# Performance work log

Hardware: AMD Instinct MI355X
Metric: run time of the kernel (lower is better)

## Reference

```python
import jax, jax.numpy as jnp
import numpy as np

EPS = 1e-06


def setup_inputs() -> dict:
    key = jax.random.key(0)
    k1, k2 = jax.random.split(key)
    x = jax.random.normal(k1, (16, 64, 256, 256), dtype=jnp.float32)
    gamma = jax.random.normal(k2, (1,), dtype=jnp.float32)
    return {"x": x, "gamma": gamma}


def reference(x, gamma):
    B, C, H, W = x.shape
    N = H * W
    v = x.reshape(B, C, N)                      # Q = K = V = flattened x
    # l2_norm: normalize across channel dim (dim=-2) per spatial position
    inv_norm = 1.0 / (jnp.linalg.norm(v, axis=1) + 1e-06)   # [B, N]
    qn = v * inv_norm[:, None, :]               # [B, C, N], Q and K normalized identically
    q_sum = jnp.sum(qn, axis=1)                 # [B, N] (sum over channels)
    # tailor_sum: 1 / (N + K^T-summed-Q + eps) -> [B, C]
    tailor = 1.0 / (N + jnp.einsum('bcn,bn->bc', qn, q_sum) + EPS)
    value_sum = jnp.sum(v, axis=1)[:, None, :]  # [B, 1, N], broadcasts over C
    matrix = jnp.einsum('bcn,bmn->bcm', v, qn)  # V @ K^T : [B, C, C]
    matrix_sum = value_sum + jnp.einsum('bcm,bmn->bcn', matrix, qn)  # [B, C, N]
    weight_value = matrix_sum * tailor[:, :, None]
    return x + gamma * weight_value.reshape(B, C, H, W)
```

## Files before the change

kernel.cpp:

```cpp
#include <hip/hip_runtime.h>
#include <stdint.h>

#define BATCH 16
#define CDIM 64
#define NDIM 65536
#define EPSV 1e-6f

typedef __attribute__((ext_vector_type(8))) short bf16x8;
typedef __attribute__((ext_vector_type(4))) short bf16x4;
typedef __attribute__((ext_vector_type(4))) float f32x4;

static __device__ __forceinline__ uint32_t f2bf(float f) {
    uint32_t u = __builtin_bit_cast(uint32_t, f);
    return (u + 0x7fffu + ((u >> 16) & 1u)) >> 16;
}
static __device__ __forceinline__ float bf2f(uint32_t h) {
    uint32_t u = h << 16;
    return __builtin_bit_cast(float, u);
}

#define T1 256
#define P1 264
#define CHUNKS 4
#define NTILE1 64

__global__ __launch_bounds__(256, 4)
void gram_kernel(const float* __restrict__ x, float* __restrict__ pmat,
                 float* __restrict__ pt) {
    __shared__ __align__(16) short ldsU[CDIM][P1];
    __shared__ __align__(16) float ldsG[T1];
    __shared__ float red[4][CDIM];

    const int tid = threadIdx.x;
    const int b = blockIdx.x >> 6;
    const int tileIdx = blockIdx.x & 63;
    const int w = tid >> 6;
    const int lane = tid & 63;
    const int cq = lane >> 4;
    const int cr = lane & 15;

    f32x4 acc0 = {0.f, 0.f, 0.f, 0.f};
    f32x4 acc1 = acc0, acc2 = acc0, acc3 = acc0;
    float tpart = 0.f;

    const float* xbase = x + (size_t)b * CDIM * NDIM;

    for (int chunk = 0; chunk < CHUNKS; ++chunk) {
        const int n0 = tileIdx * (T1 * CHUNKS) + chunk * T1;
        const float* xb = xbase + n0 + tid;
        float ss = 0.f, cs = 0.f;
#pragma unroll 8
        for (int c = 0; c < CDIM; ++c) {
            float v = xb[(size_t)c * NDIM];
            ss += v * v;
            cs += v;
            ldsU[c][tid] = (short)f2bf(v);
        }
        const float inv = 1.f / (sqrtf(ss) + EPSV);
        const float sq = sqrtf(inv);
        ldsG[tid] = inv * sq * cs;
#pragma unroll 8
        for (int c = 0; c < CDIM; ++c) {
            uint32_t h = (uint16_t)ldsU[c][tid];
            ldsU[c][tid] = (short)f2bf(bf2f(h) * sq);
        }
        __syncthreads();
#pragma unroll
        for (int ks = 0; ks < 8; ++ks) {
            const int k0 = ks * 32 + cq * 8;
            bf16x8 afrag = *(const bf16x8*)&ldsU[w * 16 + cr][k0];
            bf16x8 b0 = *(const bf16x8*)&ldsU[cr][k0];
            bf16x8 b1 = *(const bf16x8*)&ldsU[16 + cr][k0];
            bf16x8 b2 = *(const bf16x8*)&ldsU[32 + cr][k0];
            bf16x8 b3 = *(const bf16x8*)&ldsU[48 + cr][k0];
            acc0 = __builtin_amdgcn_mfma_f32_16x16x32_bf16(afrag, b0, acc0, 0, 0, 0);
            acc1 = __builtin_amdgcn_mfma_f32_16x16x32_bf16(afrag, b1, acc1, 0, 0, 0);
            acc2 = __builtin_amdgcn_mfma_f32_16x16x32_bf16(afrag, b2, acc2, 0, 0, 0);
            acc3 = __builtin_amdgcn_mfma_f32_16x16x32_bf16(afrag, b3, acc3, 0, 0, 0);
        }
#pragma unroll
        for (int i = 0; i < 8; ++i) {
            const int nb = w * 64 + i * 8;
            bf16x8 uf = *(const bf16x8*)&ldsU[lane][nb];
            f32x4 g0 = *(const f32x4*)&ldsG[nb];
            f32x4 g1 = *(const f32x4*)&ldsG[nb + 4];
#pragma unroll
            for (int j = 0; j < 4; ++j) {
                tpart += bf2f((uint32_t)(uint16_t)uf[j]) * g0[j];
                tpart += bf2f((uint32_t)(uint16_t)uf[j + 4]) * g1[j];
            }
        }
        __syncthreads();
    }
    red[w][lane] = tpart;
    __syncthreads();
    if (tid < CDIM) {
        pt[(size_t)blockIdx.x * CDIM + tid] =
            red[0][tid] + red[1][tid] + red[2][tid] + red[3][tid];
    }
    float* pm = pmat + (size_t)blockIdx.x * CDIM * CDIM;
    const f32x4 accs[4] = {acc0, acc1, acc2, acc3};
#pragma unroll
    for (int mt = 0; mt < 4; ++mt) {
#pragma unroll
        for (int r = 0; r < 4; ++r) {
            const int row = w * 16 + cq * 4 + r;
            const int col = mt * 16 + cr;
            pm[row * CDIM + col] = accs[mt][r];
        }
    }
}

__global__ __launch_bounds__(256, 4)
void reduce_kernel(const float* __restrict__ pmat, const float* __restrict__ pt,
                   float* __restrict__ mat, float* __restrict__ tl) {
    const int blk = blockIdx.x;
    const int tid = threadIdx.x;
    if (blk < 256) {
        const int b = blk >> 4;
        const int o = (blk & 15) * 256 + tid;
        float s = 0.f;
#pragma unroll 8
        for (int t = 0; t < NTILE1; ++t)
            s += pmat[((size_t)(b * NTILE1 + t)) * (CDIM * CDIM) + o];
        mat[b * CDIM * CDIM + o] = s;
    } else {
        const int idx = (blk - 256) * 256 + tid;
        const int b = idx >> 6;
        const int c = idx & 63;
        float s = 0.f;
#pragma unroll 8
        for (int t = 0; t < NTILE1; ++t)
            s += pt[(size_t)(b * NTILE1 + t) * CDIM + c];
        tl[idx] = 1.f / ((float)NDIM + s + EPSV);
    }
}

#define T2 256
#define P2 68
#define PM 72

__global__ __launch_bounds__(256, 3)
void out_kernel(const float* __restrict__ x, const float* __restrict__ mat,
                const float* __restrict__ tl, const float* __restrict__ gamma,
                float* __restrict__ out) {
    __shared__ __align__(16) short ldsV[T2][P2];
    __shared__ __align__(16) short ldsM[CDIM][PM];
    __shared__ float ldsCS[T2];
    __shared__ float ldsIN[T2];
    __shared__ float ldsTL[CDIM];

    const int tid = threadIdx.x;
    const int bid = (int)(gridDim.x - 1 - blockIdx.x);
    const int b = bid >> 8;
    const int n0 = (bid & 255) * T2;
    const int w = tid >> 6;
    const int lane = tid & 63;
    const int cq = lane >> 4;
    const int cr = lane & 15;

    const float* mb = mat + (size_t)b * CDIM * CDIM;
#pragma unroll
    for (int i = 0; i < 16; ++i) {
        const int idx = tid + i * 256;
        ldsM[idx >> 6][idx & 63] = (short)f2bf(mb[idx]);
    }
    if (tid < CDIM) ldsTL[tid] = tl[b * CDIM + tid];

    const float* xb = x + (size_t)b * CDIM * NDIM + n0 + tid;
    float ss = 0.f, cs = 0.f;
#pragma unroll 8
    for (int cp = 0; cp < 32; ++cp) {
        float v0 = xb[(size_t)(2 * cp) * NDIM];
        float v1 = xb[(size_t)(2 * cp + 1) * NDIM];
        ss += v0 * v0 + v1 * v1;
        cs += v0 + v1;
        *(uint32_t*)&ldsV[tid][2 * cp] = f2bf(v0) | (f2bf(v1) << 16);
    }
    ldsIN[tid] = 1.f / (sqrtf(ss) + EPSV);
    ldsCS[tid] = cs;
    __syncthreads();

    bf16x8 afrag[4][2];
#pragma unroll
    for (int ct = 0; ct < 4; ++ct)
#pragma unroll
        for (int ks = 0; ks < 2; ++ks)
            afrag[ct][ks] = *(const bf16x8*)&ldsM[ct * 16 + cr][ks * 32 + cq * 8];

    f32x4 acc[4][4];
#pragma unroll
    for (int p = 0; p < 4; ++p)
#pragma unroll
        for (int ct = 0; ct < 4; ++ct)
            acc[p][ct] = (f32x4){0.f, 0.f, 0.f, 0.f};

#pragma unroll
    for (int p = 0; p < 4; ++p) {
        const int n = (w * 4 + p) * 16 + cr;
#pragma unroll
        for (int ks = 0; ks < 2; ++ks) {
            const int k0 = ks * 32 + cq * 8;
            bf16x4 lo = *(const bf16x4*)&ldsV[n][k0];
            bf16x4 hi = *(const bf16x4*)&ldsV[n][k0 + 4];
            bf16x8 bfrag = __builtin_shufflevector(lo, hi, 0, 1, 2, 3, 4, 5, 6, 7);
#pragma unroll
            for (int ct = 0; ct < 4; ++ct)
                acc[p][ct] = __builtin_amdgcn_mfma_f32_16x16x32_bf16(
                    afrag[ct][ks], bfrag, acc[p][ct], 0, 0, 0);
        }
    }

    const float g = gamma[0];
    float* ob = out + (size_t)b * CDIM * NDIM + n0;
#pragma unroll
    for (int p = 0; p < 4; ++p) {
        const int n = (w * 4 + p) * 16 + cr;
        const float csn = ldsCS[n];
        const float invn = ldsIN[n];
#pragma unroll
        for (int ct = 0; ct < 4; ++ct) {
            const int c0 = ct * 16 + cq * 4;
            bf16x4 xv4 = *(const bf16x4*)&ldsV[n][c0];
#pragma unroll
            for (int r = 0; r < 4; ++r) {
                const int c = c0 + r;
                ob[(size_t)c * NDIM + n] =
                    bf2f((uint32_t)(uint16_t)xv4[r]) +
                    g * ldsTL[c] * (csn + invn * acc[p][ct][r]);
            }
        }
    }
}

extern "C" void kernel_launch(void* const* d_in, const int* in_sizes, int n_in,
                              void* d_out, int out_size, void* d_ws, size_t ws_size,
                              hipStream_t stream) {
    const float* x = (const float*)d_in[0];
    const float* gamma = (const float*)d_in[1];
    float* out = (float*)d_out;
    float* pmat = (float*)d_ws;
    float* pt = pmat + (size_t)1024 * CDIM * CDIM;
    float* mat = pt + (size_t)1024 * CDIM;
    float* tl = mat + BATCH * CDIM * CDIM;
    hipLaunchKernelGGL(gram_kernel, dim3(BATCH * NTILE1), dim3(256), 0, stream,
                       x, pmat, pt);
    hipLaunchKernelGGL(reduce_kernel, dim3(260), dim3(256), 0, stream,
                       pmat, pt, mat, tl);
    hipLaunchKernelGGL(out_kernel, dim3(BATCH * 256), dim3(256), 0, stream,
                       x, mat, tl, gamma, out);
}
```

Before: 552.4 us.

## Cache normalized fp16 U in workspace to avoid re-reading fp32 x

The gram kernel now writes the normalized, channel-contiguous fp16 U and per-position column sum and scale to workspace. The output kernel reads these instead of re-reading and re-normalizing fp32 x, reconstructing x from U. MFMA switches from bf16 to fp16, and non-temporal loads and stores are added. This cuts second-pass HBM traffic but reconstructs the residual from fp16, which loses precision, and adds extra workspace writes.

After: 534.1 us. -3.3%, faster.

```diff
diff --git a/kernel.cpp b/kernel.cpp
--- a/kernel.cpp
+++ b/kernel.cpp
@@ -6,17 +6,16 @@
 #define NDIM 65536
 #define EPSV 1e-6f
 
-typedef __attribute__((ext_vector_type(8))) short bf16x8;
-typedef __attribute__((ext_vector_type(4))) short bf16x4;
+typedef __attribute__((ext_vector_type(8))) _Float16 f16x8;
 typedef __attribute__((ext_vector_type(4))) float f32x4;
-
-static __device__ __forceinline__ uint32_t f2bf(float f) {
-    uint32_t u = __builtin_bit_cast(uint32_t, f);
-    return (u + 0x7fffu + ((u >> 16) & 1u)) >> 16;
-}
-static __device__ __forceinline__ float bf2f(uint32_t h) {
-    uint32_t u = h << 16;
-    return __builtin_bit_cast(float, u);
+typedef __attribute__((ext_vector_type(4))) uint32_t u32x4;
+typedef __attribute__((ext_vector_type(4))) short s16x4;
+
+static __device__ __forceinline__ short h2s(_Float16 h) {
+    return (short)__builtin_bit_cast(unsigned short, h);
+}
+static __device__ __forceinline__ _Float16 s2h(short s) {
+    return __builtin_bit_cast(_Float16, (unsigned short)s);
 }
 
 #define T1 256
@@ -26,7 +25,8 @@
 
 __global__ __launch_bounds__(256, 4)
 void gram_kernel(const float* __restrict__ x, float* __restrict__ pmat,
-                 float* __restrict__ pt) {
+                 float* __restrict__ pt, short* __restrict__ ut,
+                 float2* __restrict__ meta) {
     __shared__ __align__(16) short ldsU[CDIM][P1];
     __shared__ __align__(16) float ldsG[T1];
     __shared__ float red[4][CDIM];
@@ -47,47 +47,62 @@
 
     for (int chunk = 0; chunk < CHUNKS; ++chunk) {
         const int n0 = tileIdx * (T1 * CHUNKS) + chunk * T1;
-        const float* xb = xbase + n0 + tid;
+        const int n = n0 + tid;
+        const float* xb = xbase + n;
         float ss = 0.f, cs = 0.f;
 #pragma unroll 8
         for (int c = 0; c < CDIM; ++c) {
-            float v = xb[(size_t)c * NDIM];
+            float v = __builtin_nontemporal_load(xb + (size_t)c * NDIM);
             ss += v * v;
             cs += v;
-            ldsU[c][tid] = (short)f2bf(v);
+            ldsU[c][tid] = h2s((_Float16)v);
         }
         const float inv = 1.f / (sqrtf(ss) + EPSV);
         const float sq = sqrtf(inv);
+        const _Float16 sqh = (_Float16)sq;
         ldsG[tid] = inv * sq * cs;
-#pragma unroll 8
-        for (int c = 0; c < CDIM; ++c) {
-            uint32_t h = (uint16_t)ldsU[c][tid];
-            ldsU[c][tid] = (short)f2bf(bf2f(h) * sq);
+        meta[(size_t)b * NDIM + n] = make_float2(cs, (float)sqh);
+        short* urow = ut + ((size_t)b * NDIM + n) * CDIM;
+#pragma unroll
+        for (int c8 = 0; c8 < CDIM; c8 += 8) {
+            uint32_t pk0, pk1, pk2, pk3;
+#pragma unroll
+            for (int j = 0; j < 4; ++j) {
+                _Float16 u0 = s2h(ldsU[c8 + 2 * j][tid]) * sqh;
+                _Float16 u1 = s2h(ldsU[c8 + 2 * j + 1][tid]) * sqh;
+                ldsU[c8 + 2 * j][tid] = h2s(u0);
+                ldsU[c8 + 2 * j + 1][tid] = h2s(u1);
+                uint32_t p = (uint32_t)__builtin_bit_cast(unsigned short, u0) |
+                             ((uint32_t)__builtin_bit_cast(unsigned short, u1) << 16);
+                if (j == 0) pk0 = p; else if (j == 1) pk1 = p;
+                else if (j == 2) pk2 = p; else pk3 = p;
+            }
+            *(u32x4*)(urow + c8) = (u32x4){pk0, pk1, pk2, pk3};
         }
         __syncthreads();
 #pragma unroll
         for (int ks = 0; ks < 8; ++ks) {
             const int k0 = ks * 32 + cq * 8;
-            bf16x8 afrag = *(const bf16x8*)&ldsU[w * 16 + cr][k0];
-            bf16x8 b0 = *(const bf16x8*)&ldsU[cr][k0];
-            bf16x8 b1 = *(const bf16x8*)&ldsU[16 + cr][k0];
-            bf16x8 b2 = *(const bf16x8*)&ldsU[32 + cr][k0];
-            bf16x8 b3 = *(const bf16x8*)&ldsU[48 + cr][k0];
-            acc0 = __builtin_amdgcn_mfma_f32_16x16x32_bf16(afrag, b0, acc0, 0, 0, 0);
-            acc1 = __builtin_amdgcn_mfma_f32_16x16x32_bf16(afrag, b1, acc1, 0, 0, 0);
-            acc2 = __builtin_amdgcn_mfma_f32_16x16x32_bf16(afrag, b2, acc2, 0, 0, 0);
-            acc3 = __builtin_amdgcn_mfma_f32_16x16x32_bf16(afrag, b3, acc3, 0, 0, 0);
+            f16x8 afrag = *(const f16x8*)&ldsU[w * 16 + cr][k0];
+            f16x8 b0 = *(const f16x8*)&ldsU[cr][k0];
+            f16x8 b1 = *(const f16x8*)&ldsU[16 + cr][k0];
+            f16x8 b2 = *(const f16x8*)&ldsU[32 + cr][k0];
+            f16x8 b3 = *(const f16x8*)&ldsU[48 + cr][k0];
+            acc0 = __builtin_amdgcn_mfma_f32_16x16x32_f16(afrag, b0, acc0, 0, 0, 0);
+            acc1 = __builtin_amdgcn_mfma_f32_16x16x32_f16(afrag, b1, acc1, 0, 0, 0);
+            acc2 = __builtin_amdgcn_mfma_f32_16x16x32_f16(afrag, b2, acc2, 0, 0, 0);
+            acc3 = __builtin_amdgcn_mfma_f32_16x16x32_f16(afrag, b3, acc3, 0, 0, 0);
         }
 #pragma unroll
         for (int i = 0; i < 8; ++i) {
             const int nb = w * 64 + i * 8;
-            bf16x8 uf = *(const bf16x8*)&ldsU[lane][nb];
+            f16x8 uf = *(const f16x8*)&ldsU[lane][nb];
             f32x4 g0 = *(const f32x4*)&ldsG[nb];
             f32x4 g1 = *(const f32x4*)&ldsG[nb + 4];
 #pragma unroll
             for (int j = 0; j < 4; ++j) {
-                tpart += bf2f((uint32_t)(uint16_t)uf[j]) * g0[j];
-                tpart += bf2f((uint32_t)(uint16_t)uf[j + 4]) * g1[j];
+                tpart += (float)uf[j] * g0[j];
+                tpart += (float)uf[j + 4] * g1[j];
             }
         }
         __syncthreads();
@@ -113,7 +128,7 @@
 
 __global__ __launch_bounds__(256, 4)
 void reduce_kernel(const float* __restrict__ pmat, const float* __restrict__ pt,
-                   float* __restrict__ mat, float* __restrict__ tl) {
+                   short* __restrict__ matb, float* __restrict__ tl) {
     const int blk = blockIdx.x;
     const int tid = threadIdx.x;
     if (blk < 256) {
@@ -122,8 +137,9 @@
         float s = 0.f;
 #pragma unroll 8
         for (int t = 0; t < NTILE1; ++t)
-            s += pmat[((size_t)(b * NTILE1 + t)) * (CDIM * CDIM) + o];
-        mat[b * CDIM * CDIM + o] = s;
+            s += __builtin_nontemporal_load(
+                &pmat[((size_t)(b * NTILE1 + t)) * (CDIM * CDIM) + o]);
+        matb[(size_t)b * CDIM * CDIM + o] = h2s((_Float16)s);
     } else {
         const int idx = (blk - 256) * 256 + tid;
         const int b = idx >> 6;
@@ -131,62 +147,47 @@
         float s = 0.f;
 #pragma unroll 8
         for (int t = 0; t < NTILE1; ++t)
-            s += pt[(size_t)(b * NTILE1 + t) * CDIM + c];
+            s += __builtin_nontemporal_load(&pt[(size_t)(b * NTILE1 + t) * CDIM + c]);
         tl[idx] = 1.f / ((float)NDIM + s + EPSV);
     }
 }
 
-#define T2 256
-#define P2 68
 #define PM 72
 
 __global__ __launch_bounds__(256, 3)
-void out_kernel(const float* __restrict__ x, const float* __restrict__ mat,
-                const float* __restrict__ tl, const float* __restrict__ gamma,
-                float* __restrict__ out) {
-    __shared__ __align__(16) short ldsV[T2][P2];
+void out_kernel(const short* __restrict__ ut, const short* __restrict__ matb,
+                const float* __restrict__ tl, const float2* __restrict__ meta,
+                const float* __restrict__ gamma, float* __restrict__ out) {
     __shared__ __align__(16) short ldsM[CDIM][PM];
-    __shared__ float ldsCS[T2];
-    __shared__ float ldsIN[T2];
     __shared__ float ldsTL[CDIM];
 
     const int tid = threadIdx.x;
     const int bid = (int)(gridDim.x - 1 - blockIdx.x);
     const int b = bid >> 8;
-    const int n0 = (bid & 255) * T2;
+    const int n0 = (bid & 255) * 256;
     const int w = tid >> 6;
     const int lane = tid & 63;
     const int cq = lane >> 4;
     const int cr = lane & 15;
 
-    const float* mb = mat + (size_t)b * CDIM * CDIM;
-#pragma unroll
-    for (int i = 0; i < 16; ++i) {
-        const int idx = tid + i * 256;
-        ldsM[idx >> 6][idx & 63] = (short)f2bf(mb[idx]);
+    {
+        const short* mb = matb + (size_t)b * CDIM * CDIM;
+        const int c = tid >> 2;
+        const int seg = (tid & 3) * 16;
+        u32x4 q0 = *(const u32x4*)(mb + c * CDIM + seg);
+        u32x4 q1 = *(const u32x4*)(mb + c * CDIM + seg + 8);
+        *(u32x4*)&ldsM[c][seg] = q0;
+        *(u32x4*)&ldsM[c][seg + 8] = q1;
     }
     if (tid < CDIM) ldsTL[tid] = tl[b * CDIM + tid];
-
-    const float* xb = x + (size_t)b * CDIM * NDIM + n0 + tid;
-    float ss = 0.f, cs = 0.f;
-#pragma unroll 8
-    for (int cp = 0; cp < 32; ++cp) {
-        float v0 = xb[(size_t)(2 * cp) * NDIM];
-        float v1 = xb[(size_t)(2 * cp + 1) * NDIM];
-        ss += v0 * v0 + v1 * v1;
-        cs += v0 + v1;
-        *(uint32_t*)&ldsV[tid][2 * cp] = f2bf(v0) | (f2bf(v1) << 16);
-    }
-    ldsIN[tid] = 1.f / (sqrtf(ss) + EPSV);
-    ldsCS[tid] = cs;
     __syncthreads();
 
-    bf16x8 afrag[4][2];
+    f16x8 afrag[4][2];
 #pragma unroll
     for (int ct = 0; ct < 4; ++ct)
 #pragma unroll
         for (int ks = 0; ks < 2; ++ks)
-            afrag[ct][ks] = *(const bf16x8*)&ldsM[ct * 16 + cr][ks * 32 + cq * 8];
+            afrag[ct][ks] = *(const f16x8*)&ldsM[ct * 16 + cr][ks * 32 + cq * 8];
 
     f32x4 acc[4][4];
 #pragma unroll
@@ -195,39 +196,42 @@
         for (int ct = 0; ct < 4; ++ct)
             acc[p][ct] = (f32x4){0.f, 0.f, 0.f, 0.f};
 
+    const short* ub = ut + (size_t)b * NDIM * CDIM;
+
 #pragma unroll
     for (int p = 0; p < 4; ++p) {
-        const int n = (w * 4 + p) * 16 + cr;
+        const int n = n0 + (w * 4 + p) * 16 + cr;
+        const short* urow = ub + (size_t)n * CDIM;
 #pragma unroll
         for (int ks = 0; ks < 2; ++ks) {
-            const int k0 = ks * 32 + cq * 8;
-            bf16x4 lo = *(const bf16x4*)&ldsV[n][k0];
-            bf16x4 hi = *(const bf16x4*)&ldsV[n][k0 + 4];
-            bf16x8 bfrag = __builtin_shufflevector(lo, hi, 0, 1, 2, 3, 4, 5, 6, 7);
+            f16x8 bfrag = *(const f16x8*)(urow + ks * 32 + cq * 8);
 #pragma unroll
             for (int ct = 0; ct < 4; ++ct)
-                acc[p][ct] = __builtin_amdgcn_mfma_f32_16x16x32_bf16(
+                acc[p][ct] = __builtin_amdgcn_mfma_f32_16x16x32_f16(
                     afrag[ct][ks], bfrag, acc[p][ct], 0, 0, 0);
         }
     }
 
     const float g = gamma[0];
-    float* ob = out + (size_t)b * CDIM * NDIM + n0;
+    float* obase = out + (size_t)b * CDIM * NDIM;
 #pragma unroll
     for (int p = 0; p < 4; ++p) {
-        const int n = (w * 4 + p) * 16 + cr;
-        const float csn = ldsCS[n];
-        const float invn = ldsIN[n];
+        const int n = n0 + (w * 4 + p) * 16 + cr;
+        const float2 ms = meta[(size_t)b * NDIM + n];
+        const float csn = ms.x;
+        const float sn = ms.y;
+        const float rs = 1.0f / sn;
+        const short* urow = ub + (size_t)n * CDIM;
 #pragma unroll
         for (int ct = 0; ct < 4; ++ct) {
             const int c0 = ct * 16 + cq * 4;
-            bf16x4 xv4 = *(const bf16x4*)&ldsV[n][c0];
+            s16x4 uv = *(const s16x4*)(urow + c0);
 #pragma unroll
             for (int r = 0; r < 4; ++r) {
                 const int c = c0 + r;
-                ob[(size_t)c * NDIM + n] =
-                    bf2f((uint32_t)(uint16_t)xv4[r]) +
-                    g * ldsTL[c] * (csn + invn * acc[p][ct][r]);
+                float val = (float)s2h(uv[r]) * rs +
+                            g * ldsTL[c] * (csn + sn * acc[p][ct][r]);
+                __builtin_nontemporal_store(val, obase + (size_t)c * NDIM + n);
             }
         }
     }
@@ -239,14 +243,18 @@
     const float* x = (const float*)d_in[0];
     const float* gamma = (const float*)d_in[1];
     float* out = (float*)d_out;
-    float* pmat = (float*)d_ws;
+    float* ws = (float*)d_ws;
+    short* ut = (short*)ws;
+    float* pmat = ws + (size_t)33554432;
     float* pt = pmat + (size_t)1024 * CDIM * CDIM;
-    float* mat = pt + (size_t)1024 * CDIM;
-    float* tl = mat + BATCH * CDIM * CDIM;
+    float2* meta = (float2*)(pt + (size_t)1024 * CDIM);
+    short* matb = (short*)((float*)meta + (size_t)2 * BATCH * NDIM);
+    float* tl = (float*)(matb + (size_t)BATCH * CDIM * CDIM);
+
     hipLaunchKernelGGL(gram_kernel, dim3(BATCH * NTILE1), dim3(256), 0, stream,
-                       x, pmat, pt);
+                       x, pmat, pt, ut, meta);
     hipLaunchKernelGGL(reduce_kernel, dim3(260), dim3(256), 0, stream,
-                       pmat, pt, mat, tl);
+                       pmat, pt, matb, tl);
     hipLaunchKernelGGL(out_kernel, dim3(BATCH * 256), dim3(256), 0, stream,
-                       x, mat, tl, gamma, out);
-}
+                       ut, matb, tl, meta, gamma, out);
+}
```
